# Optimization experiments

Measured on AMD Instinct MI355X. Metric: run time of the kernel, lower is better.

The kernel has to match this reference:

```python
import jax, jax.numpy as jnp
import numpy as np

B, T, HID = 2, 2048, 2048
H, DQ, DV, R = 16, 128, 128, 32
DCQ, DCKV, DCO = 768, 512, 512
EPS = 1e-6
SCALE = DQ ** -0.5


def _rms(x, w):
    xf = x.astype(jnp.float32)
    var = jnp.mean(xf * xf, axis=-1, keepdims=True)
    return w * (xf * jax.lax.rsqrt(var + EPS)).astype(x.dtype)


def _rotate_half(x):
    d = x.shape[-1] // 2
    return jnp.concatenate([-x[..., d:], x[..., :d]], axis=-1)


def setup_inputs() -> dict:
    key = jax.random.key(0)
    ks = jax.random.split(key, 9)
    s = 0.02
    hidden_states = jax.random.normal(ks[0], (B, T, HID), dtype=jnp.float32)
    # RoPE tables: inv_freq over R/2 dims, duplicated (cat(freqs, freqs))
    inv_freq = 1.0 / (10000.0 ** (np.arange(0, R, 2, dtype=np.float32) / R))
    freqs = np.arange(T, dtype=np.float32)[:, None] * inv_freq[None, :]  # [T, R/2]
    emb = np.concatenate([freqs, freqs], axis=-1)  # [T, R]
    cos = jnp.asarray(np.cos(emb))
    sin = jnp.asarray(np.sin(emb))
    return {
        "hidden_states": hidden_states,
        "cos": cos,
        "sin": sin,
        "Wq_shared": jax.random.normal(ks[1], (DCQ, HID), jnp.float32) * s,
        "q_shared_norm_w": jnp.ones((DCQ,), jnp.float32),
        "Wkv_shared": jax.random.normal(ks[2], (DCKV, HID), jnp.float32) * s,
        "kv_shared_norm_w": jnp.ones((DCKV,), jnp.float32),
        "Wq_private": jax.random.normal(ks[3], (H * DQ, DCQ), jnp.float32) * s,
        "Wkv_private": jax.random.normal(ks[4], (H * (DQ + DV), DCKV), jnp.float32) * s,
        "Wg_private": jax.random.normal(ks[5], (H * DV, HID), jnp.float32) * s,
        "Wo_private": jax.random.normal(ks[6], (DCO, H * DV), jnp.float32) * s,
        "o_private_norm_w": jnp.ones((DCO,), jnp.float32),
        "Wo_shared": jax.random.normal(ks[7], (HID, DCO), jnp.float32) * s,
    }


def reference(hidden_states, cos, sin, Wq_shared, q_shared_norm_w, Wkv_shared,
              kv_shared_norm_w, Wq_private, Wkv_private, Wg_private,
              Wo_private, o_private_norm_w, Wo_shared):
    x = hidden_states
    b, t, _ = x.shape
    # shared (latent) projections + RMSNorm
    q_shared = _rms(x @ Wq_shared.T, q_shared_norm_w)    # [B,T,DCQ]
    kv_shared = _rms(x @ Wkv_shared.T, kv_shared_norm_w)  # [B,T,DCKV]
    # private per-head projections
    q = (q_shared @ Wq_private.T).reshape(b, t, H, DQ).transpose(0, 2, 1, 3)
    kv = kv_shared @ Wkv_private.T                        # [B,T,H*(DQ+DV)]
    k_flat, v_flat = jnp.split(kv, 2, axis=-1)            # keys block then values block
    gates = jax.nn.silu(x @ Wg_private.T)                 # [B,T,H*DV]
    v_flat = v_flat * gates
    k = k_flat.reshape(b, t, H, DQ).transpose(0, 2, 1, 3)
    v = v_flat.reshape(b, t, H, DV).transpose(0, 2, 1, 3)
    # partial RoPE on first R dims of each head
    c = cos[None, None]  # [1,1,T,R]
    s = sin[None, None]
    q_rope, q_pass = q[..., :R], q[..., R:]
    k_rope, k_pass = k[..., :R], k[..., R:]
    q = jnp.concatenate([q_rope * c + _rotate_half(q_rope) * s, q_pass], axis=-1)
    k = jnp.concatenate([k_rope * c + _rotate_half(k_rope) * s, k_pass], axis=-1)
    # causal attention
    scores = jnp.einsum('bhqd,bhkd->bhqk', q, k) * SCALE
    causal = jnp.tril(jnp.ones((t, t), dtype=bool))
    scores = jnp.where(causal, scores, jnp.finfo(scores.dtype).min)
    attn = jax.nn.softmax(scores, axis=-1)
    out = jnp.einsum('bhqk,bhkd->bhqd', attn, v)
    out = out.transpose(0, 2, 1, 3).reshape(b, t, H * DV)
    # output subspace: private proj -> norm -> shared proj
    out = _rms(out @ Wo_private.T, o_private_norm_w)
    return out @ Wo_shared.T
```

## Files before the change

kernel.cpp:

```cpp
#include <hip/hip_runtime.h>
#include <stdint.h>

typedef __attribute__((ext_vector_type(8))) short short8;
typedef __attribute__((ext_vector_type(4))) short sh4;
typedef __attribute__((ext_vector_type(4))) float f32x4;

__device__ __forceinline__ float bf2f(unsigned short u) {
  union { unsigned int i; float f; } v; v.i = ((unsigned int)u) << 16; return v.f;
}
__device__ __forceinline__ unsigned short f2bf(float f) {
  union { float f; unsigned int i; } v; v.f = f;
  unsigned int u = v.i;
  return (unsigned short)((u + 0x7fffu + ((u >> 16) & 1u)) >> 16);
}

#define B_SZ 2
#define T_SEQ 2048
#define NH 16
#define DH 128
#define ROPE_R 32
#define SCALE_Q 0.08838834764831845f

template <bool F>
__device__ __forceinline__ short8 ld8(const void* base, size_t idx) {
  if constexpr (F) {
    const float* p = (const float*)base + idx;
    f32x4 a = *(const f32x4*)p;
    f32x4 b = *(const f32x4*)(p + 4);
    short8 r;
    r[0] = (short)f2bf(a[0]); r[1] = (short)f2bf(a[1]);
    r[2] = (short)f2bf(a[2]); r[3] = (short)f2bf(a[3]);
    r[4] = (short)f2bf(b[0]); r[5] = (short)f2bf(b[1]);
    r[6] = (short)f2bf(b[2]); r[7] = (short)f2bf(b[3]);
    return r;
  } else {
    return *(const short8*)((const unsigned short*)base + idx);
  }
}

template <bool AF, bool BF, bool C32>
__global__ __launch_bounds__(256) void gemm_bt(
    const void* __restrict__ Ap, const void* __restrict__ Bp,
    void* __restrict__ Cp, int M, int N, int K) {
  __shared__ unsigned short Al[128][40];
  __shared__ unsigned short Bl[128][40];
  const int tid = threadIdx.x;
  const int lane = tid & 63, w = tid >> 6;
  const int wm = w >> 1, wn = w & 1;
  const int quad = lane >> 4, l16 = lane & 15;
  const int m0 = blockIdx.y * 128, n0 = blockIdx.x * 128;
  f32x4 acc[4][4];
#pragma unroll
  for (int i = 0; i < 4; ++i)
#pragma unroll
    for (int j = 0; j < 4; ++j)
#pragma unroll
      for (int r = 0; r < 4; ++r) acc[i][j][r] = 0.f;

  for (int k0 = 0; k0 < K; k0 += 32) {
    __syncthreads();
#pragma unroll
    for (int p = 0; p < 2; ++p) {
      int v = tid + p * 256;
      int row = v >> 2, kc = (v & 3) * 8;
      *(short8*)&Al[row][kc] = ld8<AF>(Ap, (size_t)(m0 + row) * K + k0 + kc);
      *(short8*)&Bl[row][kc] = ld8<BF>(Bp, (size_t)(n0 + row) * K + k0 + kc);
    }
    __syncthreads();
    short8 a[4];
#pragma unroll
    for (int i = 0; i < 4; ++i)
      a[i] = *(const short8*)&Al[wm * 64 + i * 16 + l16][quad * 8];
#pragma unroll
    for (int j = 0; j < 4; ++j) {
      short8 b = *(const short8*)&Bl[wn * 64 + j * 16 + l16][quad * 8];
#pragma unroll
      for (int i = 0; i < 4; ++i)
        acc[i][j] = __builtin_amdgcn_mfma_f32_16x16x32_bf16(a[i], b, acc[i][j], 0, 0, 0);
    }
  }
#pragma unroll
  for (int i = 0; i < 4; ++i)
#pragma unroll
    for (int j = 0; j < 4; ++j) {
      int row = m0 + wm * 64 + i * 16 + quad * 4;
      int col = n0 + wn * 64 + j * 16 + l16;
#pragma unroll
      for (int r = 0; r < 4; ++r) {
        if constexpr (C32)
          ((float*)Cp)[(size_t)(row + r) * N + col] = acc[i][j][r];
        else
          ((unsigned short*)Cp)[(size_t)(row + r) * N + col] = f2bf(acc[i][j][r]);
      }
    }
}

__device__ __forceinline__ void gload_lds16(const unsigned short* g, unsigned short* l) {
  __builtin_amdgcn_global_load_lds(
      (const __attribute__((address_space(1))) void*)g,
      (__attribute__((address_space(3))) void*)l, 16, 0, 0);
}

template <int BN, bool C32>
__global__ __launch_bounds__(256) void gemm_lds(
    const unsigned short* __restrict__ A, const unsigned short* __restrict__ Bw,
    void* __restrict__ Cp, int M, int N, int K) {
  __shared__ unsigned short Al[128][32];
  __shared__ unsigned short Bl[BN][32];
  const int tid = threadIdx.x;
  const int lane = tid & 63, w = tid >> 6;
  const int wm = w >> 1, wn = w & 1;
  const int quad = lane >> 4, l16 = lane & 15;
  const int m0 = blockIdx.y * 128, n0 = blockIdx.x * BN;
  constexpr int NJ = BN / 32;
  f32x4 acc[4][NJ];
#pragma unroll
  for (int i = 0; i < 4; ++i)
#pragma unroll
    for (int j = 0; j < NJ; ++j)
#pragma unroll
      for (int r = 0; r < 4; ++r) acc[i][j][r] = 0.f;

  for (int k0 = 0; k0 < K; k0 += 32) {
    __syncthreads();
#pragma unroll
    for (int p = 0; p < 2; ++p) {
      int c = w * 128 + p * 64 + lane;
      gload_lds16(A + (size_t)(m0 + (c >> 2)) * K + k0 + (c & 3) * 8,
                  &Al[0][0] + (size_t)(w * 128 + p * 64) * 8);
    }
#pragma unroll
    for (int p = 0; p < BN / 64; ++p) {
      int c = w * BN + p * 64 + lane;
      gload_lds16(Bw + (size_t)(n0 + (c >> 2)) * K + k0 + (c & 3) * 8,
                  &Bl[0][0] + (size_t)(w * BN + p * 64) * 8);
    }
    __syncthreads();
    short8 a[4], b[NJ];
#pragma unroll
    for (int i = 0; i < 4; ++i)
      a[i] = *(const short8*)&Al[wm * 64 + i * 16 + l16][quad * 8];
#pragma unroll
    for (int j = 0; j < NJ; ++j)
      b[j] = *(const short8*)&Bl[wn * (BN / 2) + j * 16 + l16][quad * 8];
#pragma unroll
    for (int j = 0; j < NJ; ++j)
#pragma unroll
      for (int i = 0; i < 4; ++i)
        acc[i][j] = __builtin_amdgcn_mfma_f32_16x16x32_bf16(a[i], b[j], acc[i][j], 0, 0, 0);
  }
#pragma unroll
  for (int i = 0; i < 4; ++i)
#pragma unroll
    for (int j = 0; j < NJ; ++j) {
      int row = m0 + wm * 64 + i * 16 + quad * 4;
      int col = n0 + wn * (BN / 2) + j * 16 + l16;
#pragma unroll
      for (int r = 0; r < 4; ++r) {
        if constexpr (C32)
          ((float*)Cp)[(size_t)(row + r) * N + col] = acc[i][j][r];
        else
          ((unsigned short*)Cp)[(size_t)(row + r) * N + col] = f2bf(acc[i][j][r]);
      }
    }
}

struct CvtArgs {
  const float* src[8];
  unsigned short* dst[8];
  long long n4[8];
};

__global__ __launch_bounds__(256) void cvt_multi(CvtArgs a, long long total4) {
  for (long long g = (long long)blockIdx.x * 256 + threadIdx.x; g < total4;
       g += (long long)gridDim.x * 256) {
    long long r = g;
    int s = 0;
    while (r >= a.n4[s]) { r -= a.n4[s]; ++s; }
    f32x4 v = ((const f32x4*)a.src[s])[r];
    sh4 o;
    o[0] = (short)f2bf(v[0]); o[1] = (short)f2bf(v[1]);
    o[2] = (short)f2bf(v[2]); o[3] = (short)f2bf(v[3]);
    ((sh4*)a.dst[s])[r] = o;
  }
}

__global__ __launch_bounds__(256) void rms_norm_ip(
    unsigned short* __restrict__ x, const float* __restrict__ w, int N) {
  unsigned short* row = x + (size_t)blockIdx.x * N;
  float vals[8];
  int cnt = 0;
  float ss = 0.f;
  for (int j = threadIdx.x; j < N; j += 256) {
    float v = bf2f(row[j]);
    vals[cnt++] = v;
    ss += v * v;
  }
#pragma unroll
  for (int d = 1; d < 64; d <<= 1) ss += __shfl_xor(ss, d);
  __shared__ float ws4[4];
  if ((threadIdx.x & 63) == 0) ws4[threadIdx.x >> 6] = ss;
  __syncthreads();
  float tot = ws4[0] + ws4[1] + ws4[2] + ws4[3];
  float scale = rsqrtf(tot / (float)N + 1e-6f);
  cnt = 0;
  for (int j = threadIdx.x; j < N; j += 256)
    row[j] = f2bf(w[j] * vals[cnt++] * scale);
}

__global__ __launch_bounds__(256) void prep_qk(
    const unsigned short* __restrict__ q_all, const unsigned short* __restrict__ k_all,
    const float* __restrict__ cosb, const float* __restrict__ sinb,
    unsigned short* __restrict__ Q, unsigned short* __restrict__ K) {
  const int bt = blockIdx.x;
  const int b = bt >> 11, t = bt & (T_SEQ - 1);
  const unsigned short* qr = q_all + (size_t)bt * (NH * DH);
  const unsigned short* kr = k_all + (size_t)bt * (NH * DH);
  for (int d = threadIdx.x; d < NH * DH; d += 256) {
    int h = d >> 7, dd = d & 127;
    float qv = bf2f(qr[d]);
    float kv = bf2f(kr[d]);
    if (dd < ROPE_R) {
      float c = cosb[t * ROPE_R + dd];
      float s = sinb[t * ROPE_R + dd];
      float qrot = (dd < 16) ? -bf2f(qr[d + 16]) : bf2f(qr[d - 16]);
      float krot = (dd < 16) ? -bf2f(kr[d + 16]) : bf2f(kr[d - 16]);
      qv = qv * c + qrot * s;
      kv = kv * c + krot * s;
    }
    size_t o = ((size_t)(b * NH + h) * T_SEQ + t) * DH + dd;
    Q[o] = f2bf(qv * SCALE_Q);
    K[o] = f2bf(kv);
  }
}

__global__ __launch_bounds__(256) void prep_vt(
    const unsigned short* __restrict__ v_all, const unsigned short* __restrict__ gates,
    unsigned short* __restrict__ Vt) {
  __shared__ unsigned short tile[64][130];
  const int bh = blockIdx.y, b = bh >> 4, h = bh & 15;
  const int t0 = blockIdx.x * 64;
  for (int idx = threadIdx.x; idx < 64 * 128; idx += 256) {
    int tt = idx >> 7, dd = idx & 127;
    size_t rowbase = (size_t)(b * T_SEQ + t0 + tt);
    float v = bf2f(v_all[rowbase * (NH * DH) + h * DH + dd]);
    float g = bf2f(gates[rowbase * (NH * DH) + h * DH + dd]);
    float sg = g / (1.f + __expf(-g));
    tile[tt][dd] = f2bf(v * sg);
  }
  __syncthreads();
  for (int idx = threadIdx.x; idx < 64 * 128; idx += 256) {
    int dd = idx >> 6, tt = idx & 63;
    Vt[((size_t)bh * DH + dd) * T_SEQ + t0 + tt] = tile[tt][dd];
  }
}

__device__ __forceinline__ void attn_update(
    const unsigned short* __restrict__ Kb, const unsigned short* __restrict__ Vb,
    unsigned short (*Pw)[96], const short8* qf, int qt, int kb, bool diag,
    int wt, int quad, int l16, f32x4* O, float* m_run, float* l_run) {
  f32x4 sc[4];
  __builtin_amdgcn_s_setprio(1);
#pragma unroll
  for (int jt = 0; jt < 4; ++jt) {
#pragma unroll
    for (int r = 0; r < 4; ++r) sc[jt][r] = 0.f;
#pragma unroll
    for (int kk = 0; kk < 4; ++kk) {
      short8 kf = *(const short8*)&Kb[(size_t)(kb + jt * 16 + l16) * DH + kk * 32 + quad * 8];
      sc[jt] = __builtin_amdgcn_mfma_f32_16x16x32_bf16(qf[kk], kf, sc[jt], 0, 0, 0);
    }
  }
  __builtin_amdgcn_s_setprio(0);
  if (diag) {
#pragma unroll
    for (int jt = 0; jt < 4; ++jt) {
      int key = kb + jt * 16 + l16;
#pragma unroll
      for (int r = 0; r < 4; ++r) {
        int row = qt * 64 + wt * 16 + quad * 4 + r;
        if (key > row) sc[jt][r] = -1e30f;
      }
    }
  }
  float pmax[4], psum[4];
#pragma unroll
  for (int r = 0; r < 4; ++r)
    pmax[r] = fmaxf(fmaxf(sc[0][r], sc[1][r]), fmaxf(sc[2][r], sc[3][r]));
  bool near = (pmax[0] <= m_run[0] + 8.f) & (pmax[1] <= m_run[1] + 8.f) &
              (pmax[2] <= m_run[2] + 8.f) & (pmax[3] <= m_run[3] + 8.f);
  if (__all((int)near)) {
#pragma unroll
    for (int r = 0; r < 4; ++r) psum[r] = 0.f;
#pragma unroll
    for (int jt = 0; jt < 4; ++jt)
#pragma unroll
      for (int r = 0; r < 4; ++r) {
        float p = __expf(sc[jt][r] - m_run[r]);
        sc[jt][r] = p;
        psum[r] += p;
      }
#pragma unroll
    for (int r = 0; r < 4; ++r) {
      float s = psum[r];
      s += __shfl_xor(s, 1); s += __shfl_xor(s, 2);
      s += __shfl_xor(s, 4); s += __shfl_xor(s, 8);
      l_run[r] += s;
    }
  } else {
    float alpha[4];
#pragma unroll
    for (int r = 0; r < 4; ++r) {
      float mx = pmax[r];
      mx = fmaxf(mx, __shfl_xor(mx, 1)); mx = fmaxf(mx, __shfl_xor(mx, 2));
      mx = fmaxf(mx, __shfl_xor(mx, 4)); mx = fmaxf(mx, __shfl_xor(mx, 8));
      float mnew = fmaxf(m_run[r], mx);
      alpha[r] = __expf(m_run[r] - mnew);
      m_run[r] = mnew;
      psum[r] = 0.f;
    }
#pragma unroll
    for (int jt = 0; jt < 4; ++jt)
#pragma unroll
      for (int r = 0; r < 4; ++r) {
        float p = __expf(sc[jt][r] - m_run[r]);
        sc[jt][r] = p;
        psum[r] += p;
      }
#pragma unroll
    for (int r = 0; r < 4; ++r) {
      float s = psum[r];
      s += __shfl_xor(s, 1); s += __shfl_xor(s, 2);
      s += __shfl_xor(s, 4); s += __shfl_xor(s, 8);
      l_run[r] = l_run[r] * alpha[r] + s;
    }
#pragma unroll
    for (int jn = 0; jn < 8; ++jn)
#pragma unroll
      for (int r = 0; r < 4; ++r) O[jn][r] *= alpha[r];
  }
#pragma unroll
  for (int jt = 0; jt < 4; ++jt)
#pragma unroll
    for (int r = 0; r < 4; ++r)
      Pw[quad * 4 + r][jt * 16 + l16] = f2bf(sc[jt][r]);
  short8 pa[2];
#pragma unroll
  for (int kk = 0; kk < 2; ++kk)
    pa[kk] = *(const short8*)&Pw[l16][kk * 32 + quad * 8];
  __builtin_amdgcn_s_setprio(1);
#pragma unroll
  for (int jn = 0; jn < 8; ++jn) {
#pragma unroll
    for (int kk = 0; kk < 2; ++kk) {
      short8 vf = *(const short8*)&Vb[(size_t)(jn * 16 + l16) * T_SEQ + kb + kk * 32 + quad * 8];
      O[jn] = __builtin_amdgcn_mfma_f32_16x16x32_bf16(pa[kk], vf, O[jn], 0, 0, 0);
    }
  }
  __builtin_amdgcn_s_setprio(0);
}

__global__ __launch_bounds__(512, 4) void flash_attn(
    const unsigned short* __restrict__ Q, const unsigned short* __restrict__ K,
    const unsigned short* __restrict__ Vt, unsigned short* __restrict__ Out) {
  __shared__ unsigned short P_lds[8][16][96];
  const int l = blockIdx.x;
  const int s = l & 7, qq = l >> 3;
  const int bh = s + 8 * (qq >> 4);
  const int qp = qq & 15;
  const int qa = qp, qb = 31 - qp;
  const int b = bh >> 4, h = bh & 15;
  const int tid = threadIdx.x;
  const int lane = tid & 63, w = tid >> 6;
  const int wt = w & 3;
  const bool isB = w >= 4;
  const int myq = isB ? qb : qa;
  const int quad = lane >> 4, l16 = lane & 15;
  const unsigned short* Qb = Q + (size_t)bh * T_SEQ * DH;
  const unsigned short* Kb = K + (size_t)bh * T_SEQ * DH;
  const unsigned short* Vb = Vt + (size_t)bh * DH * T_SEQ;

  short8 qf[4];
  const int qrow = myq * 64 + wt * 16 + l16;
#pragma unroll
  for (int kk = 0; kk < 4; ++kk)
    qf[kk] = *(const short8*)&Qb[(size_t)qrow * DH + kk * 32 + quad * 8];

  f32x4 O[8];
  float m_run[4], l_run[4];
#pragma unroll
  for (int jn = 0; jn < 8; ++jn)
#pragma unroll
    for (int r = 0; r < 4; ++r) O[jn][r] = 0.f;
#pragma unroll
  for (int r = 0; r < 4; ++r) { m_run[r] = -1e30f; l_run[r] = 0.f; }

  const int my_last = myq;
  for (int kt = 0; kt <= my_last; ++kt)
    attn_update(Kb, Vb, P_lds[w], qf, myq, kt * 64, kt == my_last,
                wt, quad, l16, O, m_run, l_run);

#pragma unroll
  for (int jn = 0; jn < 8; ++jn)
#pragma unroll
    for (int r = 0; r < 4; ++r) {
      int rr = myq * 64 + wt * 16 + quad * 4 + r;
      Out[((size_t)(b * T_SEQ) + rr) * (NH * DH) + h * DH + jn * 16 + l16] =
          f2bf(O[jn][r] / l_run[r]);
    }
}

extern "C" void kernel_launch(void* const* d_in, const int* in_sizes, int n_in,
                              void* d_out, int out_size, void* d_ws, size_t ws_size,
                              hipStream_t stream) {
  const void*  x     = d_in[0];
  const float* cosb  = (const float*)d_in[1];
  const float* sinb  = (const float*)d_in[2];
  const void*  Wq_s  = d_in[3];
  const float* qs_w  = (const float*)d_in[4];
  const void*  Wkv_s = d_in[5];
  const float* kvs_w = (const float*)d_in[6];
  const void*  Wq_p  = d_in[7];
  const float* Wkv_p = (const float*)d_in[8];
  const void*  Wg_p  = d_in[9];
  const void*  Wo_p  = d_in[10];
  const float* o_w   = (const float*)d_in[11];
  const void*  Wo_s  = d_in[12];
  (void)in_sizes; (void)n_in; (void)out_size;

  const int M = B_SZ * T_SEQ;
  char* ws = (char*)d_ws;
  unsigned short* qs    = (unsigned short*)(ws + 0);
  unsigned short* omid  = qs;
  unsigned short* kvs   = (unsigned short*)(ws + 6291456);
  unsigned short* gates = (unsigned short*)(ws + 10485760);
  unsigned short* k_all = gates;
  unsigned short* v_all = (unsigned short*)(ws + 27262976);
  unsigned short* Qb    = v_all;
  unsigned short* Vt    = (unsigned short*)(ws + 44040192);
  unsigned short* Kb    = (unsigned short*)(ws + 60817408);
  unsigned short* q_all = (unsigned short*)d_out;
  unsigned short* attn  = (unsigned short*)d_out;

  dim3 blk(256);
  dim3 blk512(512);
  const size_t FAST_WS_NEEDED = 119537664;

  if (ws_size >= FAST_WS_NEEDED) {
    unsigned short* xb     = (unsigned short*)(ws + 77594624);
    unsigned short* Wq_s_b = (unsigned short*)(ws + 94371840);
    unsigned short* Wkv_s_b= (unsigned short*)(ws + 97517568);
    unsigned short* Wg_p_b = (unsigned short*)(ws + 99614720);
    unsigned short* Wq_p_b = (unsigned short*)(ws + 108003328);
    unsigned short* Wkv_p_b= (unsigned short*)(ws + 111149056);
    unsigned short* Wo_p_b = (unsigned short*)(ws + 115343360);
    unsigned short* Wo_s_b = (unsigned short*)(ws + 117440512);

    CvtArgs ca;
    ca.src[0] = (const float*)x;    ca.dst[0] = xb;      ca.n4[0] = 2097152;
    ca.src[1] = (const float*)Wq_s; ca.dst[1] = Wq_s_b;  ca.n4[1] = 393216;
    ca.src[2] = (const float*)Wkv_s;ca.dst[2] = Wkv_s_b; ca.n4[2] = 262144;
    ca.src[3] = (const float*)Wg_p; ca.dst[3] = Wg_p_b;  ca.n4[3] = 1048576;
    ca.src[4] = (const float*)Wq_p; ca.dst[4] = Wq_p_b;  ca.n4[4] = 393216;
    ca.src[5] = Wkv_p;              ca.dst[5] = Wkv_p_b; ca.n4[5] = 524288;
    ca.src[6] = (const float*)Wo_p; ca.dst[6] = Wo_p_b;  ca.n4[6] = 262144;
    ca.src[7] = (const float*)Wo_s; ca.dst[7] = Wo_s_b;  ca.n4[7] = 262144;
    long long total4 = 5242880;
    cvt_multi<<<dim3(2048), blk, 0, stream>>>(ca, total4);

    gemm_lds<128, false><<<dim3(768 / 128, M / 128), blk, 0, stream>>>(xb, Wq_s_b, qs, M, 768, 2048);
    gemm_lds<64,  false><<<dim3(512 / 64,  M / 128), blk, 0, stream>>>(xb, Wkv_s_b, kvs, M, 512, 2048);
    gemm_lds<128, false><<<dim3(2048 / 128, M / 128), blk, 0, stream>>>(xb, Wg_p_b, gates, M, 2048, 2048);
    rms_norm_ip<<<M, blk, 0, stream>>>(qs, qs_w, 768);
    rms_norm_ip<<<M, blk, 0, stream>>>(kvs, kvs_w, 512);
    gemm_lds<128, false><<<dim3(2048 / 128, M / 128), blk, 0, stream>>>(qs, Wq_p_b, q_all, M, 2048, 768);
    gemm_lds<128, false><<<dim3(2048 / 128, M / 128), blk, 0, stream>>>(
        kvs, Wkv_p_b + (size_t)2048 * 512, v_all, M, 2048, 512);
    prep_vt<<<dim3(T_SEQ / 64, B_SZ * NH), blk, 0, stream>>>(v_all, gates, Vt);
    gemm_lds<128, false><<<dim3(2048 / 128, M / 128), blk, 0, stream>>>(kvs, Wkv_p_b, k_all, M, 2048, 512);
    prep_qk<<<M, blk, 0, stream>>>(q_all, k_all, cosb, sinb, Qb, Kb);
    flash_attn<<<dim3(512), blk512, 0, stream>>>(Qb, Kb, Vt, attn);
    gemm_lds<64,  false><<<dim3(512 / 64, M / 128), blk, 0, stream>>>(attn, Wo_p_b, omid, M, 512, 2048);
    rms_norm_ip<<<M, blk, 0, stream>>>(omid, o_w, 512);
    gemm_lds<128, true><<<dim3(2048 / 128, M / 128), blk, 0, stream>>>(omid, Wo_s_b, d_out, M, 2048, 512);
  } else {
    gemm_bt<true, true, false><<<dim3(768 / 128, M / 128), blk, 0, stream>>>(x, Wq_s, qs, M, 768, 2048);
    gemm_bt<true, true, false><<<dim3(512 / 128, M / 128), blk, 0, stream>>>(x, Wkv_s, kvs, M, 512, 2048);
    gemm_bt<true, true, false><<<dim3(2048 / 128, M / 128), blk, 0, stream>>>(x, Wg_p, gates, M, 2048, 2048);
    rms_norm_ip<<<M, blk, 0, stream>>>(qs, qs_w, 768);
    rms_norm_ip<<<M, blk, 0, stream>>>(kvs, kvs_w, 512);
    gemm_bt<false, true, false><<<dim3(2048 / 128, M / 128), blk, 0, stream>>>(qs, Wq_p, q_all, M, 2048, 768);
    gemm_bt<false, true, false><<<dim3(2048 / 128, M / 128), blk, 0, stream>>>(
        kvs, Wkv_p + (size_t)2048 * 512, v_all, M, 2048, 512);
    prep_vt<<<dim3(T_SEQ / 64, B_SZ * NH), blk, 0, stream>>>(v_all, gates, Vt);
    gemm_bt<false, true, false><<<dim3(2048 / 128, M / 128), blk, 0, stream>>>(kvs, Wkv_p, k_all, M, 2048, 512);
    prep_qk<<<M, blk, 0, stream>>>(q_all, k_all, cosb, sinb, Qb, Kb);
    flash_attn<<<dim3(512), blk512, 0, stream>>>(Qb, Kb, Vt, attn);
    gemm_bt<false, true, false><<<dim3(512 / 128, M / 128), blk, 0, stream>>>(attn, Wo_p, omid, M, 512, 2048);
    rms_norm_ip<<<M, blk, 0, stream>>>(omid, o_w, 512);
    gemm_bt<false, true, true><<<dim3(2048 / 128, M / 128), blk, 0, stream>>>(omid, Wo_s, d_out, M, 2048, 512);
  }
}
```

Baseline: 717.1 us.

## Restructure flash attention with register-prefetched K/V and per-tile blocks

Flash attention now runs 256-thread blocks, one 64-row query tile each (1024 blocks), in place of 512-thread blocks pairing tiles qp and 31-qp for causal load balance. K fragments for the next key tile are prefetched into registers while the current tile is processed, and V fragments are loaded early to overlap global latency with the softmax. The row-sum is kept as a per-lane partial and reduced once at the end, removing per-iteration shuffles. Costs: much higher register pressure (32 short8 buffers) that may cut occupancy or spill, and losing the paired-tile scheme may leave load imbalance across the causal triangle.

```diff
diff --git a/kernel.cpp b/kernel.cpp
--- a/kernel.cpp
+++ b/kernel.cpp
@@ -255,156 +255,147 @@
   }
 }
 
-__device__ __forceinline__ void attn_update(
-    const unsigned short* __restrict__ Kb, const unsigned short* __restrict__ Vb,
-    unsigned short (*Pw)[96], const short8* qf, int qt, int kb, bool diag,
-    int wt, int quad, int l16, f32x4* O, float* m_run, float* l_run) {
-  f32x4 sc[4];
-  __builtin_amdgcn_s_setprio(1);
-#pragma unroll
-  for (int jt = 0; jt < 4; ++jt) {
-#pragma unroll
-    for (int r = 0; r < 4; ++r) sc[jt][r] = 0.f;
-#pragma unroll
-    for (int kk = 0; kk < 4; ++kk) {
-      short8 kf = *(const short8*)&Kb[(size_t)(kb + jt * 16 + l16) * DH + kk * 32 + quad * 8];
-      sc[jt] = __builtin_amdgcn_mfma_f32_16x16x32_bf16(qf[kk], kf, sc[jt], 0, 0, 0);
-    }
-  }
-  __builtin_amdgcn_s_setprio(0);
-  if (diag) {
-#pragma unroll
-    for (int jt = 0; jt < 4; ++jt) {
-      int key = kb + jt * 16 + l16;
-#pragma unroll
-      for (int r = 0; r < 4; ++r) {
-        int row = qt * 64 + wt * 16 + quad * 4 + r;
-        if (key > row) sc[jt][r] = -1e30f;
-      }
-    }
-  }
-  float pmax[4], psum[4];
-#pragma unroll
-  for (int r = 0; r < 4; ++r)
-    pmax[r] = fmaxf(fmaxf(sc[0][r], sc[1][r]), fmaxf(sc[2][r], sc[3][r]));
-  bool near = (pmax[0] <= m_run[0] + 8.f) & (pmax[1] <= m_run[1] + 8.f) &
-              (pmax[2] <= m_run[2] + 8.f) & (pmax[3] <= m_run[3] + 8.f);
-  if (__all((int)near)) {
-#pragma unroll
-    for (int r = 0; r < 4; ++r) psum[r] = 0.f;
-#pragma unroll
-    for (int jt = 0; jt < 4; ++jt)
-#pragma unroll
-      for (int r = 0; r < 4; ++r) {
-        float p = __expf(sc[jt][r] - m_run[r]);
-        sc[jt][r] = p;
-        psum[r] += p;
-      }
-#pragma unroll
-    for (int r = 0; r < 4; ++r) {
-      float s = psum[r];
-      s += __shfl_xor(s, 1); s += __shfl_xor(s, 2);
-      s += __shfl_xor(s, 4); s += __shfl_xor(s, 8);
-      l_run[r] += s;
-    }
-  } else {
-    float alpha[4];
-#pragma unroll
-    for (int r = 0; r < 4; ++r) {
-      float mx = pmax[r];
-      mx = fmaxf(mx, __shfl_xor(mx, 1)); mx = fmaxf(mx, __shfl_xor(mx, 2));
-      mx = fmaxf(mx, __shfl_xor(mx, 4)); mx = fmaxf(mx, __shfl_xor(mx, 8));
-      float mnew = fmaxf(m_run[r], mx);
-      alpha[r] = __expf(m_run[r] - mnew);
-      m_run[r] = mnew;
-      psum[r] = 0.f;
-    }
-#pragma unroll
-    for (int jt = 0; jt < 4; ++jt)
-#pragma unroll
-      for (int r = 0; r < 4; ++r) {
-        float p = __expf(sc[jt][r] - m_run[r]);
-        sc[jt][r] = p;
-        psum[r] += p;
-      }
-#pragma unroll
-    for (int r = 0; r < 4; ++r) {
-      float s = psum[r];
-      s += __shfl_xor(s, 1); s += __shfl_xor(s, 2);
-      s += __shfl_xor(s, 4); s += __shfl_xor(s, 8);
-      l_run[r] = l_run[r] * alpha[r] + s;
-    }
-#pragma unroll
-    for (int jn = 0; jn < 8; ++jn)
-#pragma unroll
-      for (int r = 0; r < 4; ++r) O[jn][r] *= alpha[r];
-  }
-#pragma unroll
-  for (int jt = 0; jt < 4; ++jt)
-#pragma unroll
-    for (int r = 0; r < 4; ++r)
-      Pw[quad * 4 + r][jt * 16 + l16] = f2bf(sc[jt][r]);
-  short8 pa[2];
-#pragma unroll
-  for (int kk = 0; kk < 2; ++kk)
-    pa[kk] = *(const short8*)&Pw[l16][kk * 32 + quad * 8];
-  __builtin_amdgcn_s_setprio(1);
-#pragma unroll
-  for (int jn = 0; jn < 8; ++jn) {
-#pragma unroll
-    for (int kk = 0; kk < 2; ++kk) {
-      short8 vf = *(const short8*)&Vb[(size_t)(jn * 16 + l16) * T_SEQ + kb + kk * 32 + quad * 8];
-      O[jn] = __builtin_amdgcn_mfma_f32_16x16x32_bf16(pa[kk], vf, O[jn], 0, 0, 0);
-    }
-  }
-  __builtin_amdgcn_s_setprio(0);
-}
-
-__global__ __launch_bounds__(512, 4) void flash_attn(
+__global__ __launch_bounds__(256, 2) void flash_attn(
     const unsigned short* __restrict__ Q, const unsigned short* __restrict__ K,
     const unsigned short* __restrict__ Vt, unsigned short* __restrict__ Out) {
-  __shared__ unsigned short P_lds[8][16][96];
+  __shared__ unsigned short P_lds[4][16][96];
   const int l = blockIdx.x;
-  const int s = l & 7, qq = l >> 3;
-  const int bh = s + 8 * (qq >> 4);
-  const int qp = qq & 15;
-  const int qa = qp, qb = 31 - qp;
+  const int s = l & 7, rest = l >> 3;
+  const int qt = rest & 31;
+  const int bh = s + 8 * (rest >> 5);
   const int b = bh >> 4, h = bh & 15;
   const int tid = threadIdx.x;
   const int lane = tid & 63, w = tid >> 6;
-  const int wt = w & 3;
-  const bool isB = w >= 4;
-  const int myq = isB ? qb : qa;
   const int quad = lane >> 4, l16 = lane & 15;
   const unsigned short* Qb = Q + (size_t)bh * T_SEQ * DH;
   const unsigned short* Kb = K + (size_t)bh * T_SEQ * DH;
   const unsigned short* Vb = Vt + (size_t)bh * DH * T_SEQ;
+  unsigned short (*Pw)[96] = P_lds[w];
 
   short8 qf[4];
-  const int qrow = myq * 64 + wt * 16 + l16;
+  const int qrow = qt * 64 + w * 16 + l16;
 #pragma unroll
   for (int kk = 0; kk < 4; ++kk)
     qf[kk] = *(const short8*)&Qb[(size_t)qrow * DH + kk * 32 + quad * 8];
 
   f32x4 O[8];
-  float m_run[4], l_run[4];
+  float m_run[4], l_part[4];
 #pragma unroll
   for (int jn = 0; jn < 8; ++jn)
 #pragma unroll
     for (int r = 0; r < 4; ++r) O[jn][r] = 0.f;
 #pragma unroll
-  for (int r = 0; r < 4; ++r) { m_run[r] = -1e30f; l_run[r] = 0.f; }
-
-  const int my_last = myq;
-  for (int kt = 0; kt <= my_last; ++kt)
-    attn_update(Kb, Vb, P_lds[w], qf, myq, kt * 64, kt == my_last,
-                wt, quad, l16, O, m_run, l_run);
-
+  for (int r = 0; r < 4; ++r) { m_run[r] = -1e30f; l_part[r] = 0.f; }
+
+  short8 kreg[16];
+#pragma unroll
+  for (int i = 0; i < 16; ++i) {
+    const int jt = i >> 2, kk = i & 3;
+    kreg[i] = *(const short8*)&Kb[(size_t)(jt * 16 + l16) * DH + kk * 32 + quad * 8];
+  }
+
+  for (int kt = 0; kt <= qt; ++kt) {
+    const int kb = kt * 64;
+    f32x4 sc[4];
+    __builtin_amdgcn_s_setprio(1);
+#pragma unroll
+    for (int jt = 0; jt < 4; ++jt) {
+#pragma unroll
+      for (int r = 0; r < 4; ++r) sc[jt][r] = 0.f;
+#pragma unroll
+      for (int kk = 0; kk < 4; ++kk)
+        sc[jt] = __builtin_amdgcn_mfma_f32_16x16x32_bf16(qf[kk], kreg[jt * 4 + kk], sc[jt], 0, 0, 0);
+    }
+    __builtin_amdgcn_s_setprio(0);
+    short8 vreg[16];
+#pragma unroll
+    for (int i = 0; i < 16; ++i) {
+      const int jn = i >> 1, kk = i & 1;
+      vreg[i] = *(const short8*)&Vb[(size_t)(jn * 16 + l16) * T_SEQ + kb + kk * 32 + quad * 8];
+    }
+    if (kt < qt) {
+      const int nb = kb + 64;
+#pragma unroll
+      for (int i = 0; i < 16; ++i) {
+        const int jt = i >> 2, kk = i & 3;
+        kreg[i] = *(const short8*)&Kb[(size_t)(nb + jt * 16 + l16) * DH + kk * 32 + quad * 8];
+      }
+    }
+    if (kt == qt) {
+#pragma unroll
+      for (int jt = 0; jt < 4; ++jt) {
+        int key = kb + jt * 16 + l16;
+#pragma unroll
+        for (int r = 0; r < 4; ++r) {
+          int row = qt * 64 + w * 16 + quad * 4 + r;
+          if (key > row) sc[jt][r] = -1e30f;
+        }
+      }
+    }
+    float pmax[4];
+#pragma unroll
+    for (int r = 0; r < 4; ++r)
+      pmax[r] = fmaxf(fmaxf(sc[0][r], sc[1][r]), fmaxf(sc[2][r], sc[3][r]));
+    bool near = (pmax[0] <= m_run[0] + 8.f) & (pmax[1] <= m_run[1] + 8.f) &
+                (pmax[2] <= m_run[2] + 8.f) & (pmax[3] <= m_run[3] + 8.f);
+    if (!__all((int)near)) {
+      float alpha[4];
+#pragma unroll
+      for (int r = 0; r < 4; ++r) {
+        float mx = pmax[r];
+        mx = fmaxf(mx, __shfl_xor(mx, 1)); mx = fmaxf(mx, __shfl_xor(mx, 2));
+        mx = fmaxf(mx, __shfl_xor(mx, 4)); mx = fmaxf(mx, __shfl_xor(mx, 8));
+        float mnew = fmaxf(m_run[r], mx);
+        alpha[r] = __expf(m_run[r] - mnew);
+        m_run[r] = mnew;
+      }
+#pragma unroll
+      for (int r = 0; r < 4; ++r) l_part[r] *= alpha[r];
+#pragma unroll
+      for (int jn = 0; jn < 8; ++jn)
+#pragma unroll
+        for (int r = 0; r < 4; ++r) O[jn][r] *= alpha[r];
+    }
+#pragma unroll
+    for (int jt = 0; jt < 4; ++jt)
+#pragma unroll
+      for (int r = 0; r < 4; ++r) {
+        float p = __expf(sc[jt][r] - m_run[r]);
+        sc[jt][r] = p;
+        l_part[r] += p;
+      }
+#pragma unroll
+    for (int jt = 0; jt < 4; ++jt)
+#pragma unroll
+      for (int r = 0; r < 4; ++r)
+        Pw[quad * 4 + r][jt * 16 + l16] = f2bf(sc[jt][r]);
+    short8 pa[2];
+#pragma unroll
+    for (int kk = 0; kk < 2; ++kk)
+      pa[kk] = *(const short8*)&Pw[l16][kk * 32 + quad * 8];
+    __builtin_amdgcn_s_setprio(1);
+#pragma unroll
+    for (int jn = 0; jn < 8; ++jn) {
+#pragma unroll
+      for (int kk = 0; kk < 2; ++kk)
+        O[jn] = __builtin_amdgcn_mfma_f32_16x16x32_bf16(pa[kk], vreg[jn * 2 + kk], O[jn], 0, 0, 0);
+    }
+    __builtin_amdgcn_s_setprio(0);
+  }
+
+  float l_run[4];
+#pragma unroll
+  for (int r = 0; r < 4; ++r) {
+    float ssum = l_part[r];
+    ssum += __shfl_xor(ssum, 1); ssum += __shfl_xor(ssum, 2);
+    ssum += __shfl_xor(ssum, 4); ssum += __shfl_xor(ssum, 8);
+    l_run[r] = ssum;
+  }
 #pragma unroll
   for (int jn = 0; jn < 8; ++jn)
 #pragma unroll
     for (int r = 0; r < 4; ++r) {
-      int rr = myq * 64 + wt * 16 + quad * 4 + r;
+      int rr = qt * 64 + w * 16 + quad * 4 + r;
       Out[((size_t)(b * T_SEQ) + rr) * (NH * DH) + h * DH + jn * 16 + l16] =
           f2bf(O[jn][r] / l_run[r]);
     }
@@ -443,7 +434,6 @@
   unsigned short* attn  = (unsigned short*)d_out;
 
   dim3 blk(256);
-  dim3 blk512(512);
   const size_t FAST_WS_NEEDED = 119537664;
 
   if (ws_size >= FAST_WS_NEEDED) {
@@ -479,7 +469,7 @@
     prep_vt<<<dim3(T_SEQ / 64, B_SZ * NH), blk, 0, stream>>>(v_all, gates, Vt);
     gemm_lds<128, false><<<dim3(2048 / 128, M / 128), blk, 0, stream>>>(kvs, Wkv_p_b, k_all, M, 2048, 512);
     prep_qk<<<M, blk, 0, stream>>>(q_all, k_all, cosb, sinb, Qb, Kb);
-    flash_attn<<<dim3(512), blk512, 0, stream>>>(Qb, Kb, Vt, attn);
+    flash_attn<<<dim3(1024), blk, 0, stream>>>(Qb, Kb, Vt, attn);
     gemm_lds<64,  false><<<dim3(512 / 64, M / 128), blk, 0, stream>>>(attn, Wo_p_b, omid, M, 512, 2048);
     rms_norm_ip<<<M, blk, 0, stream>>>(omid, o_w, 512);
     gemm_lds<128, true><<<dim3(2048 / 128, M / 128), blk, 0, stream>>>(omid, Wo_s_b, d_out, M, 2048, 512);
@@ -495,7 +485,7 @@
     prep_vt<<<dim3(T_SEQ / 64, B_SZ * NH), blk, 0, stream>>>(v_all, gates, Vt);
     gemm_bt<false, true, false><<<dim3(2048 / 128, M / 128), blk, 0, stream>>>(kvs, Wkv_p, k_all, M, 2048, 512);
     prep_qk<<<M, blk, 0, stream>>>(q_all, k_all, cosb, sinb, Qb, Kb);
-    flash_attn<<<dim3(512), blk512, 0, stream>>>(Qb, Kb, Vt, attn);
+    flash_attn<<<dim3(1024), blk, 0, stream>>>(Qb, Kb, Vt, attn);
     gemm_bt<false, true, false><<<dim3(512 / 128, M / 128), blk, 0, stream>>>(attn, Wo_p, omid, M, 512, 2048);
     rms_norm_ip<<<M, blk, 0, stream>>>(omid, o_w, 512);
     gemm_bt<false, true, true><<<dim3(2048 / 128, M / 128), blk, 0, stream>>>(omid, Wo_s, d_out, M, 2048, 512);
```

Measured after the change: 783.7 us. 1.09x slower.
